# Optimization experiments

Measured on AMD Instinct MI355X. Metric: run time of the kernel, lower is better.

Reference implementation:

```python
import jax, jax.numpy as jnp
import numpy as np

B, S, D, H, OUT = 64, 2048, 1024, 300, 2
DROPOUT = 0.2


def setup_inputs() -> dict:
    key = jax.random.key(0)
    k_in, k_ids, k_pos, k_mask, k_w1, k_w2 = jax.random.split(key, 6)
    inputs = jax.random.normal(k_in, (B, S, D), dtype=jnp.float32)
    # token ids in [2, 32000); then plant a single '1' (EOS/pad marker) per row
    input_ids = jax.random.randint(k_ids, (B, S), 2, 32000, dtype=jnp.int64)
    eos_pos = jax.random.randint(k_pos, (B,), S // 2, S)
    input_ids = input_ids.at[jnp.arange(B), eos_pos].set(1)
    # realized Bernoulli(1 - dropout) token-keep mask, [B, S, 1]
    drop_mask = (jax.random.uniform(k_mask, (B, S, 1)) < (1.0 - DROPOUT)).astype(jnp.float32)
    W1 = jax.random.normal(k_w1, (H, D), dtype=jnp.float32) * 0.02
    b1 = jnp.zeros((H,), dtype=jnp.float32)
    W2 = jax.random.normal(k_w2, (OUT, H), dtype=jnp.float32) * 0.02
    b2 = jnp.zeros((OUT,), dtype=jnp.float32)
    return {"inputs": inputs, "input_ids": input_ids, "drop_mask": drop_mask,
            "W1": W1, "b1": b1, "W2": W2, "b2": b2}


def reference(inputs, input_ids, drop_mask, W1, b1, W2, b2):
    # end_ind[i] = first position where input_ids[i] == 1; fallback matches
    # the original's `except: end_ind = input_ids.shape[0]` (== batch size)
    is_end = input_ids == 1                              # [B, S]
    has_end = jnp.any(is_end, axis=1)                    # [B]
    first_end = jnp.argmax(is_end, axis=1)               # [B]
    end_ind = jnp.where(has_end, first_end, input_ids.shape[0])

    # masked, dropped segment-average over the first end_ind tokens
    valid = (jnp.arange(inputs.shape[1])[None, :] < end_ind[:, None])  # [B, S]
    weighted = inputs * drop_mask * valid[:, :, None].astype(inputs.dtype)
    euph = weighted.sum(axis=1) / end_ind[:, None].astype(inputs.dtype)  # [B, D]

    # 2-layer MLP with tanh
    hidden = jnp.tanh(euph @ W1.T + b1)
    out = hidden @ W2.T + b2                             # [B, 2]
    return out
```

## Files before the change

kernel.cpp:

```cpp
#include <hip/hip_runtime.h>
#include <math.h>

#define B 64
#define S 2048
#define D 1024
#define H 300
#define NOUT 2
#define NCHUNK 16
#define CHUNK_S (S / NCHUNK)

typedef float fx4 __attribute__((ext_vector_type(4)));

static __device__ __forceinline__ int imin(int a, int b) { return a < b ? a : b; }

__global__ __launch_bounds__(256) void sum_partial_kernel(
        const float* __restrict__ inputs,
        const int* __restrict__ ids,
        const float* __restrict__ drop,
        int* __restrict__ end_ind,
        float* __restrict__ partial ) {
    int chunk = blockIdx.x;
    int b = blockIdx.y;
    int t = threadIdx.x;
    int lane = t & 63;
    int widx = t >> 6;

    const int* idrow = ids + (size_t)b * S;
    int m = S;
    for (int s = t; s < S; s += 256) {
        if (idrow[s] == 1 && s < m) m = s;
    }
    #pragma unroll
    for (int off = 32; off > 0; off >>= 1) m = imin(m, __shfl_xor(m, off, 64));
    __shared__ int wmin[4];
    if (lane == 0) wmin[widx] = m;
    __syncthreads();
    int e_full = imin(imin(wmin[0], wmin[1]), imin(wmin[2], wmin[3]));
    int e = (e_full < S) ? e_full : B;
    if (t == 0 && chunk == 0) end_ind[b] = e;

    int s0 = chunk * CHUNK_S;
    int n = imin(s0 + CHUNK_S, e) - s0;

    __shared__ int   rows_l[CHUNK_S];
    __shared__ float w_l[CHUNK_S];
    __shared__ int   wcnt[2];

    float w = 0.f;
    int pos = 0;
    if (t < CHUNK_S) {
        w = (t < n) ? drop[(size_t)b * S + s0 + t] : 0.f;
        unsigned long long mask = __ballot(w != 0.f);
        pos = __popcll(mask & ((1ull << lane) - 1ull));
        if (lane == 0) wcnt[widx] = __popcll(mask);
    }
    __syncthreads();
    int base0 = (widx == 1) ? wcnt[0] : 0;
    if (t < CHUNK_S && w != 0.f) {
        rows_l[base0 + pos] = t;
        w_l[base0 + pos] = w;
    }
    int mtot = wcnt[0] + wcnt[1];
    __syncthreads();

    fx4 a0 = (fx4)(0.f);
    fx4 a1 = a0, a2 = a0, a3 = a0, a4 = a0, a5 = a0, a6 = a0, a7 = a0;

    const char* base = (const char*)inputs
                     + (((size_t)b * S + s0) * D + 4 * (size_t)t) * sizeof(float);

    int i = 0;
    for (; i + 8 <= mtot; i += 8) {
        fx4 v0 = __builtin_nontemporal_load((const fx4*)(base + ((size_t)rows_l[i + 0] << 12)));
        fx4 v1 = __builtin_nontemporal_load((const fx4*)(base + ((size_t)rows_l[i + 1] << 12)));
        fx4 v2 = __builtin_nontemporal_load((const fx4*)(base + ((size_t)rows_l[i + 2] << 12)));
        fx4 v3 = __builtin_nontemporal_load((const fx4*)(base + ((size_t)rows_l[i + 3] << 12)));
        fx4 v4 = __builtin_nontemporal_load((const fx4*)(base + ((size_t)rows_l[i + 4] << 12)));
        fx4 v5 = __builtin_nontemporal_load((const fx4*)(base + ((size_t)rows_l[i + 5] << 12)));
        fx4 v6 = __builtin_nontemporal_load((const fx4*)(base + ((size_t)rows_l[i + 6] << 12)));
        fx4 v7 = __builtin_nontemporal_load((const fx4*)(base + ((size_t)rows_l[i + 7] << 12)));
        a0 += v0 * w_l[i + 0];
        a1 += v1 * w_l[i + 1];
        a2 += v2 * w_l[i + 2];
        a3 += v3 * w_l[i + 3];
        a4 += v4 * w_l[i + 4];
        a5 += v5 * w_l[i + 5];
        a6 += v6 * w_l[i + 6];
        a7 += v7 * w_l[i + 7];
    }
    for (; i < mtot; ++i) {
        fx4 v = __builtin_nontemporal_load((const fx4*)(base + ((size_t)rows_l[i] << 12)));
        a0 += v * w_l[i];
    }
    a0 = ((a0 + a1) + (a2 + a3)) + ((a4 + a5) + (a6 + a7));

    fx4* op = (fx4*)(partial + ((size_t)b * NCHUNK + chunk) * D) + t;
    *op = a0;
}

__global__ __launch_bounds__(512) void mlp_kernel(
        const float* __restrict__ partial,
        const int* __restrict__ end_ind,
        const float* __restrict__ W1, const float* __restrict__ b1,
        const float* __restrict__ W2, const float* __restrict__ b2,
        float* __restrict__ out) {
    int b = blockIdx.x;
    int t = threadIdx.x;
    int wave = t >> 6;
    int lane = t & 63;

    __shared__ fx4 x4[D / 4];
    __shared__ float hidden[H];
    __shared__ float red[512];

    float inv_e = 1.0f / (float)end_ind[b];
    if (t < D / 4) {
        fx4 a = (fx4)(0.f);
        const fx4* p = (const fx4*)(partial + (size_t)b * NCHUNK * D) + t;
        for (int c = 0; c < NCHUNK; ++c, p += D / 4) {
            a += p[0];
        }
        x4[t] = a * inv_e;
    }
    __syncthreads();

    fx4 xr0 = x4[lane];
    fx4 xr1 = x4[lane + 64];
    fx4 xr2 = x4[lane + 128];
    fx4 xr3 = x4[lane + 192];

    for (int h = wave; h < H; h += 8) {
        const fx4* w = (const fx4*)(W1 + (size_t)h * D);
        fx4 acc = xr0 * w[lane]
                + xr1 * w[lane + 64]
                + xr2 * w[lane + 128]
                + xr3 * w[lane + 192];
        float d = acc.x + acc.y + acc.z + acc.w;
        #pragma unroll
        for (int mm = 32; mm > 0; mm >>= 1) d += __shfl_xor(d, mm, 64);
        if (lane == 0) hidden[h] = tanhf(d + b1[h]);
    }
    __syncthreads();

    for (int o = 0; o < NOUT; ++o) {
        float p = 0.f;
        for (int h = t; h < H; h += 512) p += hidden[h] * W2[(size_t)o * H + h];
        red[t] = p;
        __syncthreads();
        for (int st = 256; st > 0; st >>= 1) {
            if (t < st) red[t] += red[t + st];
            __syncthreads();
        }
        if (t == 0) out[b * NOUT + o] = red[0] + b2[o];
        __syncthreads();
    }
}

extern "C" void kernel_launch(void* const* d_in, const int* in_sizes, int n_in,
                              void* d_out, int out_size, void* d_ws, size_t ws_size,
                              hipStream_t stream) {
    const float* inputs = (const float*)d_in[0];
    const int*   ids    = (const int*)d_in[1];
    const float* drop   = (const float*)d_in[2];
    const float* W1     = (const float*)d_in[3];
    const float* b1v    = (const float*)d_in[4];
    const float* W2     = (const float*)d_in[5];
    const float* b2v    = (const float*)d_in[6];
    float* out = (float*)d_out;

    int*   end_ind = (int*)d_ws;
    float* partial = (float*)((char*)d_ws + 256);

    sum_partial_kernel<<<dim3(NCHUNK, B), 256, 0, stream>>>(inputs, ids, drop, end_ind, partial);
    mlp_kernel<<<B, 512, 0, stream>>>(partial, end_ind, W1, b1v, W2, b2v, out);
}
```

Before: 667.6 us.

## Compact kept rows per batch and split them evenly across chunk blocks

Adds a separate compaction kernel that finds the end index and builds a per-batch list of kept row indices and weights. The sum kernel then splits each batch's kept rows evenly across 16 blocks, instead of using fixed sequence chunks where blocks past the end index had no work. This is meant to remove load imbalance and idle blocks. The cost is an extra kernel launch and a workspace round trip for the compacted lists. The grid ordering also changes to (B, NCHUNK).

```diff
diff --git a/kernel.cpp b/kernel.cpp
--- a/kernel.cpp
+++ b/kernel.cpp
@@ -7,20 +7,19 @@
 #define H 300
 #define NOUT 2
 #define NCHUNK 16
-#define CHUNK_S (S / NCHUNK)
 
 typedef float fx4 __attribute__((ext_vector_type(4)));
 
 static __device__ __forceinline__ int imin(int a, int b) { return a < b ? a : b; }
 
-__global__ __launch_bounds__(256) void sum_partial_kernel(
-        const float* __restrict__ inputs,
+__global__ __launch_bounds__(256) void compact_kernel(
         const int* __restrict__ ids,
         const float* __restrict__ drop,
         int* __restrict__ end_ind,
-        float* __restrict__ partial ) {
-    int chunk = blockIdx.x;
-    int b = blockIdx.y;
+        int* __restrict__ cnt,
+        unsigned short* __restrict__ srows ,
+        float* __restrict__ sw ) {
+    int b = blockIdx.x;
     int t = threadIdx.x;
     int lane = t & 63;
     int widx = t >> 6;
@@ -37,40 +36,78 @@
     __syncthreads();
     int e_full = imin(imin(wmin[0], wmin[1]), imin(wmin[2], wmin[3]));
     int e = (e_full < S) ? e_full : B;
-    if (t == 0 && chunk == 0) end_ind[b] = e;
-
-    int s0 = chunk * CHUNK_S;
-    int n = imin(s0 + CHUNK_S, e) - s0;
-
-    __shared__ int   rows_l[CHUNK_S];
-    __shared__ float w_l[CHUNK_S];
-    __shared__ int   wcnt[2];
-
-    float w = 0.f;
-    int pos = 0;
-    if (t < CHUNK_S) {
-        w = (t < n) ? drop[(size_t)b * S + s0 + t] : 0.f;
-        unsigned long long mask = __ballot(w != 0.f);
-        pos = __popcll(mask & ((1ull << lane) - 1ull));
-        if (lane == 0) wcnt[widx] = __popcll(mask);
-    }
-    __syncthreads();
-    int base0 = (widx == 1) ? wcnt[0] : 0;
-    if (t < CHUNK_S && w != 0.f) {
-        rows_l[base0 + pos] = t;
-        w_l[base0 + pos] = w;
-    }
-    int mtot = wcnt[0] + wcnt[1];
+    if (t == 0) end_ind[b] = e;
+
+    __shared__ int segcnt[32];
+    __shared__ int segoff[33];
+    const float* dr = drop + (size_t)b * S;
+
+    float wv[8];
+    int pos[8];
+    bool pr[8];
+    #pragma unroll
+    for (int k = 0; k < 8; ++k) {
+        int seg = widx * 8 + k;
+        int s = seg * 64 + lane;
+        float w = dr[s];
+        bool p = (s < e) && (w != 0.f);
+        unsigned long long mask = __ballot(p);
+        wv[k] = w;
+        pr[k] = p;
+        pos[k] = __popcll(mask & ((1ull << lane) - 1ull));
+        if (lane == 0) segcnt[seg] = __popcll(mask);
+    }
+    __syncthreads();
+    if (t == 0) {
+        int acc = 0;
+        for (int i = 0; i < 32; ++i) { segoff[i] = acc; acc += segcnt[i]; }
+        segoff[32] = acc;
+        cnt[b] = acc;
+    }
+    __syncthreads();
+    #pragma unroll
+    for (int k = 0; k < 8; ++k) {
+        if (pr[k]) {
+            int seg = widx * 8 + k;
+            int s = seg * 64 + lane;
+            int o = segoff[seg] + pos[k];
+            srows[(size_t)b * S + o] = (unsigned short)s;
+            sw[(size_t)b * S + o] = wv[k];
+        }
+    }
+}
+
+__global__ __launch_bounds__(256) void sum_partial_kernel(
+        const float* __restrict__ inputs,
+        const int* __restrict__ cnt,
+        const unsigned short* __restrict__ srows,
+        const float* __restrict__ sw,
+        float* __restrict__ partial ) {
+    int b = blockIdx.x;
+    int j = blockIdx.y;
+    int t = threadIdx.x;
+
+    int c = cnt[b];
+    int lo = (j * c) >> 4;
+    int hi = ((j + 1) * c) >> 4;
+    int n = hi - lo;
+
+    __shared__ unsigned short rows_l[128];
+    __shared__ float w_l[128];
+    if (t < n) {
+        rows_l[t] = srows[(size_t)b * S + lo + t];
+        w_l[t] = sw[(size_t)b * S + lo + t];
+    }
     __syncthreads();
 
     fx4 a0 = (fx4)(0.f);
     fx4 a1 = a0, a2 = a0, a3 = a0, a4 = a0, a5 = a0, a6 = a0, a7 = a0;
 
     const char* base = (const char*)inputs
-                     + (((size_t)b * S + s0) * D + 4 * (size_t)t) * sizeof(float);
+                     + ((size_t)b * S * D + 4 * (size_t)t) * sizeof(float);
 
     int i = 0;
-    for (; i + 8 <= mtot; i += 8) {
+    for (; i + 8 <= n; i += 8) {
         fx4 v0 = __builtin_nontemporal_load((const fx4*)(base + ((size_t)rows_l[i + 0] << 12)));
         fx4 v1 = __builtin_nontemporal_load((const fx4*)(base + ((size_t)rows_l[i + 1] << 12)));
         fx4 v2 = __builtin_nontemporal_load((const fx4*)(base + ((size_t)rows_l[i + 2] << 12)));
@@ -88,13 +125,13 @@
         a6 += v6 * w_l[i + 6];
         a7 += v7 * w_l[i + 7];
     }
-    for (; i < mtot; ++i) {
+    for (; i < n; ++i) {
         fx4 v = __builtin_nontemporal_load((const fx4*)(base + ((size_t)rows_l[i] << 12)));
         a0 += v * w_l[i];
     }
     a0 = ((a0 + a1) + (a2 + a3)) + ((a4 + a5) + (a6 + a7));
 
-    fx4* op = (fx4*)(partial + ((size_t)b * NCHUNK + chunk) * D) + t;
+    fx4* op = (fx4*)(partial + ((size_t)b * NCHUNK + j) * D) + t;
     *op = a0;
 }
 
@@ -168,9 +205,13 @@
     const float* b2v    = (const float*)d_in[6];
     float* out = (float*)d_out;
 
-    int*   end_ind = (int*)d_ws;
-    float* partial = (float*)((char*)d_ws + 256);
-
-    sum_partial_kernel<<<dim3(NCHUNK, B), 256, 0, stream>>>(inputs, ids, drop, end_ind, partial);
+    int*            end_ind = (int*)d_ws;
+    int*            cnt     = (int*)((char*)d_ws + 256);
+    unsigned short* srows   = (unsigned short*)((char*)d_ws + 4096);
+    float*          sw      = (float*)((char*)d_ws + 266240);
+    float*          partial = (float*)((char*)d_ws + 790528);
+
+    compact_kernel<<<B, 256, 0, stream>>>(ids, drop, end_ind, cnt, srows, sw);
+    sum_partial_kernel<<<dim3(B, NCHUNK), 256, 0, stream>>>(inputs, cnt, srows, sw, partial);
     mlp_kernel<<<B, 512, 0, stream>>>(partial, end_ind, W1, b1v, W2, b2v, out);
 }
```

Result: no change. 671.6 us (+0.6%).
